# Kernel tuning notes

Measured on AMD Instinct MI355X. Metric: run time of the kernel, lower is better.

Reference implementation:

```python
import jax, jax.numpy as jnp
import numpy as np

NEG = -1000000000.0  # matches torch masked_fill value


def setup_inputs() -> dict:
    key = jax.random.key(0)
    ks = jax.random.split(key, 9)
    B, L, E = 2, 2048, 1024
    s = 0.02
    return {
        "query": jax.random.normal(ks[0], (B, L, E), dtype=jnp.float32),
        "w_q_w": jax.random.normal(ks[1], (E, E), dtype=jnp.float32) * s,
        "w_q_b": jax.random.normal(ks[2], (E,), dtype=jnp.float32) * s,
        "w_k_w": jax.random.normal(ks[3], (E, E), dtype=jnp.float32) * s,
        "w_k_b": jax.random.normal(ks[4], (E,), dtype=jnp.float32) * s,
        "w_v_w": jax.random.normal(ks[5], (E, E), dtype=jnp.float32) * s,
        "w_v_b": jax.random.normal(ks[6], (E,), dtype=jnp.float32) * s,
        "w_o_w": jax.random.normal(ks[7], (E, E), dtype=jnp.float32) * s,
        "w_o_b": jax.random.normal(ks[8], (E,), dtype=jnp.float32) * s,
    }


def reference(query, w_q_w, w_q_b, w_k_w, w_k_b, w_v_w, w_v_b, w_o_w, w_o_b):
    # self-attention: key = value = query (forward passes None for key/value)
    B, L, E = query.shape
    H = 16
    d_k = E // H
    scale = 1.0 / jnp.sqrt(jnp.float32(d_k))

    def proj(x, w, b):
        # torch Linear: x @ w.T + b ; then split heads -> [B, H, L, d_k]
        return (x @ w.T + b).reshape(B, L, H, d_k).transpose(0, 2, 1, 3)

    Q = proj(query, w_q_w, w_q_b)
    K = proj(query, w_k_w, w_k_b)
    V = proj(query, w_v_w, w_v_b)

    # full L x S score matrix, as in the eager original
    scores = jnp.einsum('bhqd,bhkd->bhqk', Q, K) * scale
    # causal attn_bias: upper triangle filled with -1e9 (is_causal=True path)
    causal = jnp.tril(jnp.ones((L, L), dtype=bool))
    scores = scores + jnp.where(causal, 0.0, NEG).astype(scores.dtype)
    # softmax, clear_nan (nan -> 0), + 1e-12 epsilon; dropout_p = 0.0 (no-op)
    attn = jnp.nan_to_num(jax.nn.softmax(scores, axis=-1), nan=0.0) + 1e-12

    ctx = jnp.einsum('bhqk,bhkd->bhqd', attn, V)  # [B,H,L,d_k]
    ctx = ctx.transpose(0, 2, 1, 3).reshape(B, L, E)
    return ctx @ w_o_w.T + w_o_b
```

## Files before the change

### kernel.cpp

```cpp
#include <hip/hip_runtime.h>
#include <hip/hip_bf16.h>
#include <math.h>

typedef __bf16 bf16;
typedef __bf16 bf16x4 __attribute__((ext_vector_type(4)));
typedef __bf16 bf16x8 __attribute__((ext_vector_type(8)));
typedef float  f32x4  __attribute__((ext_vector_type(4)));
typedef float  float4v __attribute__((ext_vector_type(4)));
typedef unsigned short u16x4 __attribute__((ext_vector_type(4)));

#define MFMA(a,b,c) __builtin_amdgcn_mfma_f32_16x16x32_bf16((a),(b),(c),0,0,0)

#define QSCALE 0.18033688011112042f
#define EXP2(x) __builtin_amdgcn_exp2f(x)

__device__ __forceinline__ void gload16(const bf16* g, bf16* l) {
  __builtin_amdgcn_global_load_lds(
      (const __attribute__((address_space(1))) void*)g,
      (__attribute__((address_space(3))) void*)l, 16, 0, 0);
}

__device__ __forceinline__ int detect_f32(const unsigned short* __restrict__ p) {
  int bad = 0;
  #pragma unroll
  for (int j = 0; j < 32; ++j) {
    const float x = __uint_as_float(((unsigned)p[j]) << 16);
    bad |= !(fabsf(x) <= 0.5f);
  }
  return bad;
}

__global__ void cvt_all_kernel(const void* x, const void* wq, const void* wk,
                               const void* wv, const void* wo,
                               const void* bq, const void* bk, const void* bv,
                               const void* bo,
                               bf16* cX, bf16* cWq, bf16* cWk, bf16* cWv,
                               bf16* cWo, bf16* cB)
{
  const int isf = detect_f32((const unsigned short*)bq);
  const int NX = 1048576, NW = 262144, NB = 256;
  const int total = NX + 4 * NW + 4 * NB;
  for (int gid = blockIdx.x * blockDim.x + threadIdx.x; gid < total;
       gid += gridDim.x * blockDim.x) {
    const void* s; bf16* d; int off;
    if (gid < NX)                { s = x;  d = cX;  off = gid; }
    else if (gid < NX + NW)      { s = wq; d = cWq; off = gid - NX; }
    else if (gid < NX + 2 * NW)  { s = wk; d = cWk; off = gid - NX - NW; }
    else if (gid < NX + 3 * NW)  { s = wv; d = cWv; off = gid - NX - 2 * NW; }
    else if (gid < NX + 4 * NW)  { s = wo; d = cWo; off = gid - NX - 3 * NW; }
    else {
      const int r = gid - NX - 4 * NW;
      const int wb = r / NB; off = r % NB;
      s = (wb == 0) ? bq : (wb == 1) ? bk : (wb == 2) ? bv : bo;
      d = cB + wb * 1024;
    }
    float4v v;
    if (isf) v = ((const float4v*)s)[off];
    else {
      u16x4 u = ((const u16x4*)s)[off];
      v = (float4v){__uint_as_float((unsigned)u.x << 16),
                    __uint_as_float((unsigned)u.y << 16),
                    __uint_as_float((unsigned)u.z << 16),
                    __uint_as_float((unsigned)u.w << 16)};
    }
    bf16x4 ov = {(bf16)v.x, (bf16)v.y, (bf16)v.z, (bf16)v.w};
    *(bf16x4*)&d[off * 4] = ov;
  }
}

static __device__ __forceinline__ void gemm128_core(
    const bf16* __restrict__ X, const bf16* __restrict__ W,
    int bm, int bn, f32x4 acc[4][4])
{
  __shared__ __align__(16) bf16 Als[128][64];
  __shared__ __align__(16) bf16 Bls[128][64];
  const int t    = threadIdx.x;
  const int lane = t & 63;
  const int w    = t >> 6;
  const int wr   = w >> 1, wc = w & 1;
  const int fr   = lane & 15;
  const int fq   = lane >> 4;
  const int lrow = lane >> 3;
  const int lcol = (lane & 7) * 8;

  #pragma unroll
  for (int m = 0; m < 4; ++m)
    #pragma unroll
    for (int n = 0; n < 4; ++n)
      acc[m][n] = (f32x4){0.f, 0.f, 0.f, 0.f};

  for (int k0 = 0; k0 < 1024; k0 += 64) {
    __syncthreads();
    #pragma unroll
    for (int p = 0; p < 4; ++p) {
      const int rb = p * 32 + w * 8;
      gload16(&X[(size_t)(bm + rb + lrow) * 1024 + k0 + lcol], &Als[rb][0]);
      gload16(&W[(size_t)(bn + rb + lrow) * 1024 + k0 + lcol], &Bls[rb][0]);
    }
    __syncthreads();
    #pragma unroll
    for (int kk = 0; kk < 64; kk += 32) {
      bf16x8 a[4], b[4];
      #pragma unroll
      for (int m = 0; m < 4; ++m)
        a[m] = *(const bf16x8*)&Als[wr * 64 + m * 16 + fr][kk + fq * 8];
      #pragma unroll
      for (int n = 0; n < 4; ++n)
        b[n] = *(const bf16x8*)&Bls[wc * 64 + n * 16 + fr][kk + fq * 8];
      __builtin_amdgcn_s_setprio(1);
      #pragma unroll
      for (int m = 0; m < 4; ++m)
        #pragma unroll
        for (int n = 0; n < 4; ++n)
          acc[m][n] = MFMA(a[m], b[n], acc[m][n]);
      __builtin_amdgcn_s_setprio(0);
    }
  }
}

__global__ __launch_bounds__(256, 3) void qkv_kernel(
    const bf16* __restrict__ X,
    const bf16* __restrict__ Wq, const bf16* __restrict__ Wk,
    const bf16* __restrict__ Wv, const bf16* __restrict__ Bias,
    bf16* __restrict__ Qo, bf16* __restrict__ Ko, bf16* __restrict__ Vto)
{
  const bf16 *W, *bias;
  bf16 *out;
  const int z = blockIdx.z;
  if (z == 0)      { W = Wq; bias = Bias;        out = Qo;  }
  else if (z == 1) { W = Wk; bias = Bias + 1024; out = Ko;  }
  else             { W = Wv; bias = Bias + 2048; out = Vto; }

  const int bm = blockIdx.x * 128, bn = blockIdx.y * 128;
  f32x4 acc[4][4];
  gemm128_core(X, W, bm, bn, acc);

  const int t = threadIdx.x, lane = t & 63, w = t >> 6;
  const int wr = w >> 1, wc = w & 1;
  const int fr = lane & 15, fq = lane >> 4;
  const float qs = (z == 0) ? QSCALE : 1.0f;

  #pragma unroll
  for (int n = 0; n < 4; ++n) {
    const int col = bn + wc * 64 + n * 16 + fr;
    const float bb = (float)bias[col];
    const int h = col >> 6, d = col & 63;
    if (z != 2) {
      #pragma unroll
      for (int m = 0; m < 4; ++m)
        #pragma unroll
        for (int r = 0; r < 4; ++r) {
          const int row = bm + wr * 64 + m * 16 + fq * 4 + r;
          const int b = row >> 11, li = row & 2047;
          out[(size_t)((b * 16 + h) * 2048 + li) * 64 + d] =
              (bf16)((acc[m][n][r] + bb) * qs);
        }
    } else {
      #pragma unroll
      for (int m = 0; m < 4; ++m) {
        const int tok0 = bm + wr * 64 + m * 16 + fq * 4;
        const int b = tok0 >> 11, li0 = tok0 & 2047;
        bf16x4 pk = {(bf16)(acc[m][n][0] + bb), (bf16)(acc[m][n][1] + bb),
                     (bf16)(acc[m][n][2] + bb), (bf16)(acc[m][n][3] + bb)};
        *(bf16x4*)&out[(size_t)((b * 16 + h) * 64 + d) * 2048 + li0] = pk;
      }
    }
  }
}

__device__ __forceinline__ f32x4 fmax4(f32x4 a, f32x4 b) {
  return (f32x4){fmaxf(a[0], b[0]), fmaxf(a[1], b[1]),
                 fmaxf(a[2], b[2]), fmaxf(a[3], b[3])};
}

__global__ __launch_bounds__(512, 4) void attn_kernel(
    const bf16* __restrict__ Q, const bf16* __restrict__ K,
    const bf16* __restrict__ Vt, bf16* __restrict__ CTX)
{
  const int bx = (int)blockIdx.x;
  const int gen = bx >> 8;
  const int u = bx & 255;
  const int bh = u >> 3;
  const int j = u & 7;
  const int qt = gen ? j : 15 - j;

  const int t = threadIdx.x, lane = t & 63, w = t >> 6;
  const int fr = lane & 15, fq = lane >> 4;
  const bf16* Qb = Q  + (size_t)bh * 2048 * 64;
  const bf16* Kb = K  + (size_t)bh * 2048 * 64;
  const bf16* Vb = Vt + (size_t)bh * 64 * 2048;
  const int q0 = qt * 128 + w * 16;
  const int myq = q0 + fr;
  const int nt = 2 * qt + 2;

  __shared__ __align__(16) bf16 Kls[2][64][64];
  __shared__ __align__(16) bf16 Vls[2][64][64];
  __shared__ __align__(16) bf16 Pls[8][16][64];

  const int X7   = (fr & 7) << 4;
  const int off0 = fr * 128 + ((fq * 16) ^ X7);
  const int off1 = fr * 128 + ((64 + fq * 16) ^ X7);
  const char* Kb0 = (const char*)Kls;
  const char* Vb0 = (const char*)Vls;
  char* Pw = (char*)Pls + w * 2048 + fr * 128;
  int pwoff[4];
  #pragma unroll
  for (int g = 0; g < 4; ++g) pwoff[g] = ((g * 32 + fq * 8) ^ X7);
  const int proff0 = ((fq * 16) ^ X7);
  const int proff1 = ((64 + fq * 16) ^ X7);

  const int r8 = lane >> 3;
  const int cb = (lane & 7) << 4;
  const int sc = (cb ^ (r8 << 4)) >> 1;
  const bf16* gk = Kb + (size_t)(w * 8 + r8) * 64 + sc;
  const bf16* gv = Vb + (size_t)(w * 8 + r8) * 2048 + sc;

  const bf16x8 qf0 = *(const bf16x8*)&Qb[(size_t)(q0 + fr) * 64 + fq * 8];
  const bf16x8 qf1 = *(const bf16x8*)&Qb[(size_t)(q0 + fr) * 64 + 32 + fq * 8];

  f32x4 o[4];
  #pragma unroll
  for (int g = 0; g < 4; ++g) o[g] = (f32x4){0.f, 0.f, 0.f, 0.f};
  float m_r = -1e30f;
  float s_part = 0.f;

  gload16(gk, &Kls[0][w * 8][0]);
  gload16(gv, &Vls[0][w * 8][0]);
  gk += 4096; gv += 64;
  __syncthreads();
  int cur = 0;

  for (int kt = 0; kt < nt; ++kt) {
    if (kt + 1 < nt) {
      gload16(gk, &Kls[cur ^ 1][w * 8][0]);
      gload16(gv, &Vls[cur ^ 1][w * 8][0]);
      gk += 4096; gv += 64;
    }

    const int kbase = kt * 64;
    if (kbase <= q0 + 15) {
      const char* kb = Kb0 + (cur << 13);
      const char* vb = Vb0 + (cur << 13);

      f32x4 S[4];
      __builtin_amdgcn_s_setprio(1);
      #pragma unroll
      for (int g = 0; g < 4; ++g) {
        bf16x8 kf0 = *(const bf16x8*)(kb + off0 + g * 2048);
        bf16x8 kf1 = *(const bf16x8*)(kb + off1 + g * 2048);
        f32x4 s = (f32x4){0.f, 0.f, 0.f, 0.f};
        s = MFMA(kf0, qf0, s);
        s = MFMA(kf1, qf1, s);
        S[g] = s;
      }
      __builtin_amdgcn_s_setprio(0);

      if (kbase + 63 > q0) {
        #pragma unroll
        for (int g = 0; g < 4; ++g)
          #pragma unroll
          for (int r = 0; r < 4; ++r)
            S[g][r] = (kbase + g * 16 + fq * 4 + r <= myq) ? S[g][r] : -1e9f;
      }
      f32x4 mv = fmax4(fmax4(S[0], S[1]), fmax4(S[2], S[3]));
      const float mxl = fmaxf(fmaxf(mv[0], mv[1]), fmaxf(mv[2], mv[3]));
      if (!__all(mxl <= m_r + 8.f)) {
        float mxq = fmaxf(mxl, __shfl_xor(mxl, 16));
        mxq = fmaxf(mxq, __shfl_xor(mxq, 32));
        const float mnew = fmaxf(m_r, mxq);
        const float f = EXP2(m_r - mnew);
        m_r = mnew;
        s_part *= f;
        float frow[4];
        #pragma unroll
        for (int r = 0; r < 4; ++r) frow[r] = __shfl(f, fq * 4 + r, 64);
        #pragma unroll
        for (int g = 0; g < 4; ++g)
          #pragma unroll
          for (int r = 0; r < 4; ++r) o[g][r] *= frow[r];
      }
      #pragma unroll
      for (int g = 0; g < 4; ++g)
        #pragma unroll
        for (int r = 0; r < 4; ++r) {
          const float p = EXP2(S[g][r] - m_r);
          S[g][r] = p;
          s_part += p;
        }
      #pragma unroll
      for (int g = 0; g < 4; ++g) {
        bf16x4 pk = {(bf16)S[g][0], (bf16)S[g][1], (bf16)S[g][2],
                     (bf16)S[g][3]};
        *(bf16x4*)(Pw + pwoff[g]) = pk;
      }
      __builtin_amdgcn_s_setprio(1);
      {
        bf16x8 pa0 = *(const bf16x8*)(Pw + proff0);
        #pragma unroll
        for (int g2 = 0; g2 < 4; ++g2) {
          bf16x8 vf = *(const bf16x8*)(vb + off0 + g2 * 2048);
          o[g2] = MFMA(pa0, vf, o[g2]);
        }
        bf16x8 pa1 = *(const bf16x8*)(Pw + proff1);
        #pragma unroll
        for (int g2 = 0; g2 < 4; ++g2) {
          bf16x8 vf = *(const bf16x8*)(vb + off1 + g2 * 2048);
          o[g2] = MFMA(pa1, vf, o[g2]);
        }
      }
      __builtin_amdgcn_s_setprio(0);
    }
    __syncthreads();
    cur ^= 1;
  }

  float s_r = s_part;
  s_r += __shfl_xor(s_r, 16);
  s_r += __shfl_xor(s_r, 32);
  const float inv = __builtin_amdgcn_rcpf(fmaxf(s_r, 1e-30f));
  float invr[4];
  #pragma unroll
  for (int r = 0; r < 4; ++r) invr[r] = __shfl(inv, fq * 4 + r, 64);
  const int b = bh >> 4, h = bh & 15;
  #pragma unroll
  for (int r = 0; r < 4; ++r) {
    const int tok = b * 2048 + q0 + fq * 4 + r;
    #pragma unroll
    for (int g2 = 0; g2 < 4; ++g2)
      CTX[(size_t)tok * 1024 + h * 64 + g2 * 16 + fr] =
          (bf16)(o[g2][r] * invr[r]);
  }
}

__global__ __launch_bounds__(256, 4) void out_kernel(
    const bf16* __restrict__ CTXi, const bf16* __restrict__ Wo,
    const bf16* __restrict__ bo, void* __restrict__ Y,
    const unsigned short* __restrict__ det)
{
  __shared__ __align__(16) bf16 Als[128][64];
  __shared__ __align__(16) bf16 Bls[64][64];
  const int isf = detect_f32(det);
  const int bm = blockIdx.x * 128, bn = blockIdx.y * 64;
  const int t = threadIdx.x, lane = t & 63, w = t >> 6;
  const int wr = w >> 1, wc = w & 1;
  const int fr = lane & 15, fq = lane >> 4;
  const int lrow = lane >> 3;
  const int lcol = (lane & 7) * 8;

  f32x4 acc[4][2];
  #pragma unroll
  for (int m = 0; m < 4; ++m)
    #pragma unroll
    for (int n = 0; n < 2; ++n)
      acc[m][n] = (f32x4){0.f, 0.f, 0.f, 0.f};

  for (int k0 = 0; k0 < 1024; k0 += 64) {
    __syncthreads();
    #pragma unroll
    for (int p = 0; p < 4; ++p) {
      const int rb = p * 32 + w * 8;
      gload16(&CTXi[(size_t)(bm + rb + lrow) * 1024 + k0 + lcol], &Als[rb][0]);
    }
    #pragma unroll
    for (int p = 0; p < 2; ++p) {
      const int rb = w * 16 + p * 8;
      gload16(&Wo[(size_t)(bn + rb + lrow) * 1024 + k0 + lcol], &Bls[rb][0]);
    }
    __syncthreads();
    #pragma unroll
    for (int kk = 0; kk < 64; kk += 32) {
      bf16x8 a[4], b[2];
      #pragma unroll
      for (int m = 0; m < 4; ++m)
        a[m] = *(const bf16x8*)&Als[wr * 64 + m * 16 + fr][kk + fq * 8];
      #pragma unroll
      for (int n = 0; n < 2; ++n)
        b[n] = *(const bf16x8*)&Bls[wc * 32 + n * 16 + fr][kk + fq * 8];
      __builtin_amdgcn_s_setprio(1);
      #pragma unroll
      for (int m = 0; m < 4; ++m)
        #pragma unroll
        for (int n = 0; n < 2; ++n)
          acc[m][n] = MFMA(a[m], b[n], acc[m][n]);
      __builtin_amdgcn_s_setprio(0);
    }
  }

  #pragma unroll
  for (int n = 0; n < 2; ++n) {
    const int col = bn + wc * 32 + n * 16 + fr;
    const float bb = (float)bo[col];
    #pragma unroll
    for (int m = 0; m < 4; ++m)
      #pragma unroll
      for (int r = 0; r < 4; ++r) {
        const int row = bm + wr * 64 + m * 16 + fq * 4 + r;
        const size_t idx = (size_t)row * 1024 + col;
        const float v = acc[m][n][r] + bb;
        if (isf) ((float*)Y)[idx] = v;
        else     ((bf16*)Y)[idx] = (bf16)v;
      }
  }
}

extern "C" void kernel_launch(void* const* d_in, const int* in_sizes, int n_in,
                              void* d_out, int out_size, void* d_ws, size_t ws_size,
                              hipStream_t stream) {
  char* ws = (char*)d_ws;
  const size_t MB = 1024 * 1024;

  bf16* cX  = (bf16*)(ws + 1 * MB);
  bf16* cWq = (bf16*)(ws + 9 * MB);
  bf16* cWk = (bf16*)(ws + 11 * MB);
  bf16* cWv = (bf16*)(ws + 13 * MB);
  bf16* cWo = (bf16*)(ws + 15 * MB);
  bf16* cB  = (bf16*)(ws + 17 * MB);
  bf16* Qw  = (bf16*)(ws + 18 * MB);
  bf16* Kw  = (bf16*)(ws + 26 * MB);
  bf16* Vt  = (bf16*)(ws + 34 * MB);
  bf16* CT  = (bf16*)(ws + 42 * MB);

  cvt_all_kernel<<<2048, 256, 0, stream>>>(d_in[0], d_in[1], d_in[3], d_in[5],
                                           d_in[7], d_in[2], d_in[4], d_in[6],
                                           d_in[8], cX, cWq, cWk, cWv, cWo, cB);

  qkv_kernel<<<dim3(32, 8, 3), 256, 0, stream>>>(cX, cWq, cWk, cWv, cB,
                                                 Qw, Kw, Vt);
  attn_kernel<<<512, 512, 0, stream>>>(Qw, Kw, Vt, CT);
  out_kernel<<<dim3(32, 16), 256, 0, stream>>>(CT, cWo, cB + 3072, d_out,
                                               (const unsigned short*)d_in[2]);
}
```

Before: 111.6 us.

## Split long causal attention rows across two blocks and merge partials

The attention kernel now uses 256-thread blocks over 64-query tiles. The 18 longest query tiles per head have their key range split in half across two blocks, which write unnormalized bf16 partial outputs plus running max and sum into workspace that is no longer needed. A new merge kernel rescales and combines the two partials into the context tensor. The aim is to shorten the critical path of the heaviest causal tiles and balance load across CUs, at the cost of an extra launch, partial-buffer traffic and bf16 rounding of the partials.

```diff
diff --git a/kernel.cpp b/kernel.cpp
--- a/kernel.cpp
+++ b/kernel.cpp
@@ -13,6 +13,9 @@
 
 #define QSCALE 0.18033688011112042f
 #define EXP2(x) __builtin_amdgcn_exp2f(x)
+
+#define PART_O_OFF   (1048576ull)
+#define PART_S_OFF   (1048576ull + 9437184ull)
 
 __device__ __forceinline__ void gload16(const bf16* g, bf16* l) {
   __builtin_amdgcn_global_load_lds(
@@ -173,29 +176,41 @@
                  fmaxf(a[2], b[2]), fmaxf(a[3], b[3])};
 }
 
-__global__ __launch_bounds__(512, 4) void attn_kernel(
+__global__ __launch_bounds__(256, 4) void attn_kernel(
     const bf16* __restrict__ Q, const bf16* __restrict__ K,
-    const bf16* __restrict__ Vt, bf16* __restrict__ CTX)
+    const bf16* __restrict__ Vt, bf16* __restrict__ CTX,
+    char* __restrict__ part)
 {
-  const int bx = (int)blockIdx.x;
-  const int gen = bx >> 8;
-  const int u = bx & 255;
-  const int bh = u >> 3;
-  const int j = u & 7;
-  const int qt = gen ? j : 15 - j;
+  const int id = (int)blockIdx.x;
+  int qt, bh, k0t, k1t, heavy;
+  if (id < 1152) {
+    const int pair = id >> 1, chunk = id & 1;
+    qt = 31 - (pair >> 5);
+    bh = pair & 31;
+    const int n = qt + 1, h = (n + 1) >> 1;
+    k0t = chunk ? h : 0;
+    k1t = chunk ? n : h;
+    heavy = 1;
+  } else {
+    const int r = id - 1152;
+    qt = 13 - (r >> 5);
+    bh = r & 31;
+    k0t = 0;
+    k1t = qt + 1;
+    heavy = 0;
+  }
 
   const int t = threadIdx.x, lane = t & 63, w = t >> 6;
   const int fr = lane & 15, fq = lane >> 4;
   const bf16* Qb = Q  + (size_t)bh * 2048 * 64;
   const bf16* Kb = K  + (size_t)bh * 2048 * 64;
   const bf16* Vb = Vt + (size_t)bh * 64 * 2048;
-  const int q0 = qt * 128 + w * 16;
+  const int q0 = qt * 64 + w * 16;
   const int myq = q0 + fr;
-  const int nt = 2 * qt + 2;
 
   __shared__ __align__(16) bf16 Kls[2][64][64];
   __shared__ __align__(16) bf16 Vls[2][64][64];
-  __shared__ __align__(16) bf16 Pls[8][16][64];
+  __shared__ __align__(16) bf16 Pls[4][16][64];
 
   const int X7   = (fr & 7) << 4;
   const int off0 = fr * 128 + ((fq * 16) ^ X7);
@@ -212,8 +227,10 @@
   const int r8 = lane >> 3;
   const int cb = (lane & 7) << 4;
   const int sc = (cb ^ (r8 << 4)) >> 1;
-  const bf16* gk = Kb + (size_t)(w * 8 + r8) * 64 + sc;
-  const bf16* gv = Vb + (size_t)(w * 8 + r8) * 2048 + sc;
+  const bf16* gk0 = Kb + (size_t)(k0t * 64 + w * 8 + r8) * 64 + sc;
+  const bf16* gk1 = gk0 + 32 * 64;
+  const bf16* gv0 = Vb + (size_t)(w * 8 + r8) * 2048 + k0t * 64 + sc;
+  const bf16* gv1 = gv0 + (size_t)32 * 2048;
 
   const bf16x8 qf0 = *(const bf16x8*)&Qb[(size_t)(q0 + fr) * 64 + fq * 8];
   const bf16x8 qf1 = *(const bf16x8*)&Qb[(size_t)(q0 + fr) * 64 + 32 + fq * 8];
@@ -224,92 +241,94 @@
   float m_r = -1e30f;
   float s_part = 0.f;
 
-  gload16(gk, &Kls[0][w * 8][0]);
-  gload16(gv, &Vls[0][w * 8][0]);
-  gk += 4096; gv += 64;
+  gload16(gk0, &Kls[0][w * 8][0]);
+  gload16(gk1, &Kls[0][32 + w * 8][0]);
+  gload16(gv0, &Vls[0][w * 8][0]);
+  gload16(gv1, &Vls[0][32 + w * 8][0]);
+  gk0 += 4096; gk1 += 4096; gv0 += 64; gv1 += 64;
   __syncthreads();
   int cur = 0;
 
-  for (int kt = 0; kt < nt; ++kt) {
-    if (kt + 1 < nt) {
-      gload16(gk, &Kls[cur ^ 1][w * 8][0]);
-      gload16(gv, &Vls[cur ^ 1][w * 8][0]);
-      gk += 4096; gv += 64;
-    }
-
-    const int kbase = kt * 64;
-    if (kbase <= q0 + 15) {
-      const char* kb = Kb0 + (cur << 13);
-      const char* vb = Vb0 + (cur << 13);
-
-      f32x4 S[4];
-      __builtin_amdgcn_s_setprio(1);
-      #pragma unroll
-      for (int g = 0; g < 4; ++g) {
-        bf16x8 kf0 = *(const bf16x8*)(kb + off0 + g * 2048);
-        bf16x8 kf1 = *(const bf16x8*)(kb + off1 + g * 2048);
-        f32x4 s = (f32x4){0.f, 0.f, 0.f, 0.f};
-        s = MFMA(kf0, qf0, s);
-        s = MFMA(kf1, qf1, s);
-        S[g] = s;
-      }
-      __builtin_amdgcn_s_setprio(0);
-
-      if (kbase + 63 > q0) {
-        #pragma unroll
-        for (int g = 0; g < 4; ++g)
-          #pragma unroll
-          for (int r = 0; r < 4; ++r)
-            S[g][r] = (kbase + g * 16 + fq * 4 + r <= myq) ? S[g][r] : -1e9f;
-      }
-      f32x4 mv = fmax4(fmax4(S[0], S[1]), fmax4(S[2], S[3]));
-      const float mxl = fmaxf(fmaxf(mv[0], mv[1]), fmaxf(mv[2], mv[3]));
-      if (!__all(mxl <= m_r + 8.f)) {
-        float mxq = fmaxf(mxl, __shfl_xor(mxl, 16));
-        mxq = fmaxf(mxq, __shfl_xor(mxq, 32));
-        const float mnew = fmaxf(m_r, mxq);
-        const float f = EXP2(m_r - mnew);
-        m_r = mnew;
-        s_part *= f;
-        float frow[4];
-        #pragma unroll
-        for (int r = 0; r < 4; ++r) frow[r] = __shfl(f, fq * 4 + r, 64);
-        #pragma unroll
-        for (int g = 0; g < 4; ++g)
-          #pragma unroll
-          for (int r = 0; r < 4; ++r) o[g][r] *= frow[r];
-      }
+  for (int kt = k0t; kt < k1t; ++kt) {
+    if (kt + 1 < k1t) {
+      bf16 (*Kn)[64] = Kls[cur ^ 1];
+      bf16 (*Vn)[64] = Vls[cur ^ 1];
+      gload16(gk0, &Kn[w * 8][0]);
+      gload16(gk1, &Kn[32 + w * 8][0]);
+      gload16(gv0, &Vn[w * 8][0]);
+      gload16(gv1, &Vn[32 + w * 8][0]);
+      gk0 += 4096; gk1 += 4096; gv0 += 64; gv1 += 64;
+    }
+
+    const char* kb = Kb0 + (cur << 13);
+    const char* vb = Vb0 + (cur << 13);
+
+    f32x4 S[4];
+    __builtin_amdgcn_s_setprio(1);
+    #pragma unroll
+    for (int g = 0; g < 4; ++g) {
+      bf16x8 kf0 = *(const bf16x8*)(kb + off0 + g * 2048);
+      bf16x8 kf1 = *(const bf16x8*)(kb + off1 + g * 2048);
+      f32x4 s = (f32x4){0.f, 0.f, 0.f, 0.f};
+      s = MFMA(kf0, qf0, s);
+      s = MFMA(kf1, qf1, s);
+      S[g] = s;
+    }
+    __builtin_amdgcn_s_setprio(0);
+
+    if (kt == qt) {
       #pragma unroll
       for (int g = 0; g < 4; ++g)
         #pragma unroll
-        for (int r = 0; r < 4; ++r) {
-          const float p = EXP2(S[g][r] - m_r);
-          S[g][r] = p;
-          s_part += p;
-        }
-      #pragma unroll
-      for (int g = 0; g < 4; ++g) {
-        bf16x4 pk = {(bf16)S[g][0], (bf16)S[g][1], (bf16)S[g][2],
-                     (bf16)S[g][3]};
-        *(bf16x4*)(Pw + pwoff[g]) = pk;
+        for (int r = 0; r < 4; ++r)
+          S[g][r] = (kt * 64 + g * 16 + fq * 4 + r <= myq) ? S[g][r] : -1e9f;
+    }
+    f32x4 mv = fmax4(fmax4(S[0], S[1]), fmax4(S[2], S[3]));
+    const float mxl = fmaxf(fmaxf(mv[0], mv[1]), fmaxf(mv[2], mv[3]));
+    if (!__all(mxl <= m_r + 8.f)) {
+      float mxq = fmaxf(mxl, __shfl_xor(mxl, 16));
+      mxq = fmaxf(mxq, __shfl_xor(mxq, 32));
+      const float mnew = fmaxf(m_r, mxq);
+      const float f = EXP2(m_r - mnew);
+      m_r = mnew;
+      s_part *= f;
+      float frow[4];
+      #pragma unroll
+      for (int r = 0; r < 4; ++r) frow[r] = __shfl(f, fq * 4 + r, 64);
+      #pragma unroll
+      for (int g = 0; g < 4; ++g)
+        #pragma unroll
+        for (int r = 0; r < 4; ++r) o[g][r] *= frow[r];
+    }
+    #pragma unroll
+    for (int g = 0; g < 4; ++g)
+      #pragma unroll
+      for (int r = 0; r < 4; ++r) {
+        const float p = EXP2(S[g][r] - m_r);
+        S[g][r] = p;
+        s_part += p;
       }
-      __builtin_amdgcn_s_setprio(1);
-      {
-        bf16x8 pa0 = *(const bf16x8*)(Pw + proff0);
-        #pragma unroll
-        for (int g2 = 0; g2 < 4; ++g2) {
-          bf16x8 vf = *(const bf16x8*)(vb + off0 + g2 * 2048);
-          o[g2] = MFMA(pa0, vf, o[g2]);
-        }
-        bf16x8 pa1 = *(const bf16x8*)(Pw + proff1);
-        #pragma unroll
-        for (int g2 = 0; g2 < 4; ++g2) {
-          bf16x8 vf = *(const bf16x8*)(vb + off1 + g2 * 2048);
-          o[g2] = MFMA(pa1, vf, o[g2]);
-        }
+    #pragma unroll
+    for (int g = 0; g < 4; ++g) {
+      bf16x4 pk = {(bf16)S[g][0], (bf16)S[g][1], (bf16)S[g][2], (bf16)S[g][3]};
+      *(bf16x4*)(Pw + pwoff[g]) = pk;
+    }
+    __builtin_amdgcn_s_setprio(1);
+    {
+      bf16x8 pa0 = *(const bf16x8*)(Pw + proff0);
+      #pragma unroll
+      for (int g2 = 0; g2 < 4; ++g2) {
+        bf16x8 vf = *(const bf16x8*)(vb + off0 + g2 * 2048);
+        o[g2] = MFMA(pa0, vf, o[g2]);
       }
-      __builtin_amdgcn_s_setprio(0);
-    }
+      bf16x8 pa1 = *(const bf16x8*)(Pw + proff1);
+      #pragma unroll
+      for (int g2 = 0; g2 < 4; ++g2) {
+        bf16x8 vf = *(const bf16x8*)(vb + off1 + g2 * 2048);
+        o[g2] = MFMA(pa1, vf, o[g2]);
+      }
+    }
+    __builtin_amdgcn_s_setprio(0);
     __syncthreads();
     cur ^= 1;
   }
@@ -317,18 +336,74 @@
   float s_r = s_part;
   s_r += __shfl_xor(s_r, 16);
   s_r += __shfl_xor(s_r, 32);
-  const float inv = __builtin_amdgcn_rcpf(fmaxf(s_r, 1e-30f));
-  float invr[4];
-  #pragma unroll
-  for (int r = 0; r < 4; ++r) invr[r] = __shfl(inv, fq * 4 + r, 64);
+
+  if (heavy) {
+    char* op = part + PART_O_OFF + (size_t)id * 8192 + t * 32;
+    #pragma unroll
+    for (int g2 = 0; g2 < 4; ++g2) {
+      bf16x4 pk = {(bf16)o[g2][0], (bf16)o[g2][1], (bf16)o[g2][2],
+                   (bf16)o[g2][3]};
+      *(bf16x4*)(op + g2 * 8) = pk;
+    }
+    float2 st = {m_r, s_r};
+    *(float2*)(part + PART_S_OFF + (size_t)id * 2048 + t * 8) = st;
+  } else {
+    const float inv = __builtin_amdgcn_rcpf(fmaxf(s_r, 1e-30f));
+    float invr[4];
+    #pragma unroll
+    for (int r = 0; r < 4; ++r) invr[r] = __shfl(inv, fq * 4 + r, 64);
+    const int b = bh >> 4, h = bh & 15;
+    #pragma unroll
+    for (int r = 0; r < 4; ++r) {
+      const int tok = b * 2048 + q0 + fq * 4 + r;
+      #pragma unroll
+      for (int g2 = 0; g2 < 4; ++g2)
+        CTX[(size_t)tok * 1024 + h * 64 + g2 * 16 + fr] =
+            (bf16)(o[g2][r] * invr[r]);
+    }
+  }
+}
+
+__global__ __launch_bounds__(256, 8) void merge_kernel(
+    const char* __restrict__ part, bf16* __restrict__ CTX)
+{
+  const int bi = (int)blockIdx.x;
+  const int qt = 31 - (bi >> 5), bh = bi & 31;
+  const int t = threadIdx.x, lane = t & 63, w = t >> 6;
+  const int fr = lane & 15, fq = lane >> 4;
+  const int s0 = bi * 2, s1 = s0 + 1;
+
+  const float2 st0 = *(const float2*)(part + PART_S_OFF + (size_t)s0 * 2048 + t * 8);
+  const float2 st1 = *(const float2*)(part + PART_S_OFF + (size_t)s1 * 2048 + t * 8);
+  const float M  = fmaxf(st0.x, st1.x);
+  const float f0 = EXP2(st0.x - M);
+  const float f1 = EXP2(st1.x - M);
+  const float ssum = st0.y * f0 + st1.y * f1;
+  const float inv = __builtin_amdgcn_rcpf(fmaxf(ssum, 1e-30f));
+  const float a0 = f0 * inv, a1 = f1 * inv;
+
+  float a0r[4], a1r[4];
+  #pragma unroll
+  for (int r = 0; r < 4; ++r) {
+    a0r[r] = __shfl(a0, fq * 4 + r, 64);
+    a1r[r] = __shfl(a1, fq * 4 + r, 64);
+  }
+
+  const char* o0p = part + PART_O_OFF + (size_t)s0 * 8192 + t * 32;
+  const char* o1p = part + PART_O_OFF + (size_t)s1 * 8192 + t * 32;
+
   const int b = bh >> 4, h = bh & 15;
-  #pragma unroll
-  for (int r = 0; r < 4; ++r) {
-    const int tok = b * 2048 + q0 + fq * 4 + r;
-    #pragma unroll
-    for (int g2 = 0; g2 < 4; ++g2)
-      CTX[(size_t)tok * 1024 + h * 64 + g2 * 16 + fr] =
-          (bf16)(o[g2][r] * invr[r]);
+  const int q0 = qt * 64 + w * 16;
+  #pragma unroll
+  for (int g2 = 0; g2 < 4; ++g2) {
+    bf16x4 p0 = *(const bf16x4*)(o0p + g2 * 8);
+    bf16x4 p1 = *(const bf16x4*)(o1p + g2 * 8);
+    #pragma unroll
+    for (int r = 0; r < 4; ++r) {
+      const float v = (float)p0[r] * a0r[r] + (float)p1[r] * a1r[r];
+      const int tok = b * 2048 + q0 + fq * 4 + r;
+      CTX[(size_t)tok * 1024 + h * 64 + g2 * 16 + fr] = (bf16)v;
+    }
   }
 }
 
@@ -426,7 +501,8 @@
 
   qkv_kernel<<<dim3(32, 8, 3), 256, 0, stream>>>(cX, cWq, cWk, cWv, cB,
                                                  Qw, Kw, Vt);
-  attn_kernel<<<512, 512, 0, stream>>>(Qw, Kw, Vt, CT);
+  attn_kernel<<<1600, 256, 0, stream>>>(Qw, Kw, Vt, CT, ws);
+  merge_kernel<<<576, 256, 0, stream>>>(ws, CT);
   out_kernel<<<dim3(32, 16), 256, 0, stream>>>(CT, cWo, cB + 3072, d_out,
                                                (const unsigned short*)d_in[2]);
 }
```

After: 113.7 us. About the same (+1.9%).

## Rewrite attention with 32x32 MFMA, register-resident P, and smaller blocks

Applied to the files above, without the earlier changes.

The attention kernel now uses 32x32x16 bf16 MFMA with each wave owning 32 query rows, and blocks shrink to 2 waves covering 64 queries, which doubles the grid to 1024 blocks. The softmax probabilities are repacked in registers with cvt_pk_bf16 and a cross-half lane shuffle instead of going through an LDS round-trip. Causal tile skipping is handled per 32-key half. Work balancing is reordered over four generations of query tiles. This cuts LDS traffic and per-key-tile overhead but raises register pressure and shuffle work, and each block now stages K/V for fewer queries.

```diff
diff --git a/kernel.cpp b/kernel.cpp
--- a/kernel.cpp
+++ b/kernel.cpp
@@ -6,10 +6,13 @@
 typedef __bf16 bf16x4 __attribute__((ext_vector_type(4)));
 typedef __bf16 bf16x8 __attribute__((ext_vector_type(8)));
 typedef float  f32x4  __attribute__((ext_vector_type(4)));
+typedef float  f32x16 __attribute__((ext_vector_type(16)));
 typedef float  float4v __attribute__((ext_vector_type(4)));
 typedef unsigned short u16x4 __attribute__((ext_vector_type(4)));
-
-#define MFMA(a,b,c) __builtin_amdgcn_mfma_f32_16x16x32_bf16((a),(b),(c),0,0,0)
+typedef unsigned int   u32x4 __attribute__((ext_vector_type(4)));
+
+#define MFMA16(a,b,c) __builtin_amdgcn_mfma_f32_16x16x32_bf16((a),(b),(c),0,0,0)
+#define MFMA32(a,b,c) __builtin_amdgcn_mfma_f32_32x32x16_bf16((a),(b),(c),0,0,0)
 
 #define QSCALE 0.18033688011112042f
 #define EXP2(x) __builtin_amdgcn_exp2f(x)
@@ -18,6 +21,12 @@
   __builtin_amdgcn_global_load_lds(
       (const __attribute__((address_space(1))) void*)g,
       (__attribute__((address_space(3))) void*)l, 16, 0, 0);
+}
+
+__device__ __forceinline__ unsigned cvt_pk_bf16(float lo, float hi) {
+  unsigned r;
+  asm("v_cvt_pk_bf16_f32 %0, %1, %2" : "=v"(r) : "v"(lo), "v"(hi));
+  return r;
 }
 
 __device__ __forceinline__ int detect_f32(const unsigned short* __restrict__ p) {
@@ -112,7 +121,7 @@
       for (int m = 0; m < 4; ++m)
         #pragma unroll
         for (int n = 0; n < 4; ++n)
-          acc[m][n] = MFMA(a[m], b[n], acc[m][n]);
+          acc[m][n] = MFMA16(a[m], b[n], acc[m][n]);
       __builtin_amdgcn_s_setprio(0);
     }
   }
@@ -168,12 +177,7 @@
   }
 }
 
-__device__ __forceinline__ f32x4 fmax4(f32x4 a, f32x4 b) {
-  return (f32x4){fmaxf(a[0], b[0]), fmaxf(a[1], b[1]),
-                 fmaxf(a[2], b[2]), fmaxf(a[3], b[3])};
-}
-
-__global__ __launch_bounds__(512, 4) void attn_kernel(
+__global__ __launch_bounds__(128, 3) void attn_kernel(
     const bf16* __restrict__ Q, const bf16* __restrict__ K,
     const bf16* __restrict__ Vt, bf16* __restrict__ CTX)
 {
@@ -182,153 +186,220 @@
   const int u = bx & 255;
   const int bh = u >> 3;
   const int j = u & 7;
-  const int qt = gen ? j : 15 - j;
+  int qt;
+  if (gen == 0)      qt = 31 - j;
+  else if (gen == 1) qt = 16 + j;
+  else if (gen == 2) qt = 15 - j;
+  else               qt = j;
 
   const int t = threadIdx.x, lane = t & 63, w = t >> 6;
-  const int fr = lane & 15, fq = lane >> 4;
+  const int l31 = lane & 31, ishi = lane >> 5;
   const bf16* Qb = Q  + (size_t)bh * 2048 * 64;
   const bf16* Kb = K  + (size_t)bh * 2048 * 64;
   const bf16* Vb = Vt + (size_t)bh * 64 * 2048;
-  const int q0 = qt * 128 + w * 16;
-  const int myq = q0 + fr;
-  const int nt = 2 * qt + 2;
+  const int q0w = qt * 64 + w * 32;
+  const int myq = q0w + l31;
+  const int nt = qt + 1;
+  const int hi4 = ishi * 4;
 
   __shared__ __align__(16) bf16 Kls[2][64][64];
   __shared__ __align__(16) bf16 Vls[2][64][64];
-  __shared__ __align__(16) bf16 Pls[8][16][64];
-
-  const int X7   = (fr & 7) << 4;
-  const int off0 = fr * 128 + ((fq * 16) ^ X7);
-  const int off1 = fr * 128 + ((64 + fq * 16) ^ X7);
-  const char* Kb0 = (const char*)Kls;
-  const char* Vb0 = (const char*)Vls;
-  char* Pw = (char*)Pls + w * 2048 + fr * 128;
-  int pwoff[4];
-  #pragma unroll
-  for (int g = 0; g < 4; ++g) pwoff[g] = ((g * 32 + fq * 8) ^ X7);
-  const int proff0 = ((fq * 16) ^ X7);
-  const int proff1 = ((64 + fq * 16) ^ X7);
+
+  const int koff[16] = {0,1,2,3, 8,9,10,11, 16,17,18,19, 24,25,26,27};
+
+  const int X7 = (l31 & 7) << 4;
+  const char* Kbase = (const char*)Kls + (size_t)l31 * 128;
+  const char* Vbase = (const char*)Vls + (size_t)l31 * 128;
+  int kcol[4];
+  #pragma unroll
+  for (int c = 0; c < 4; ++c) kcol[c] = (32 * c + 16 * ishi) ^ X7;
+  int vcol[2][2];
+  #pragma unroll
+  for (int kt2 = 0; kt2 < 2; ++kt2)
+    #pragma unroll
+    for (int ch = 0; ch < 2; ++ch)
+      vcol[kt2][ch] = (kt2 * 64 + ch * 32 + 16 * ishi) ^ X7;
 
   const int r8 = lane >> 3;
-  const int cb = (lane & 7) << 4;
-  const int sc = (cb ^ (r8 << 4)) >> 1;
-  const bf16* gk = Kb + (size_t)(w * 8 + r8) * 64 + sc;
-  const bf16* gv = Vb + (size_t)(w * 8 + r8) * 2048 + sc;
-
-  const bf16x8 qf0 = *(const bf16x8*)&Qb[(size_t)(q0 + fr) * 64 + fq * 8];
-  const bf16x8 qf1 = *(const bf16x8*)&Qb[(size_t)(q0 + fr) * 64 + 32 + fq * 8];
-
-  f32x4 o[4];
-  #pragma unroll
-  for (int g = 0; g < 4; ++g) o[g] = (f32x4){0.f, 0.f, 0.f, 0.f};
-  float m_r = -1e30f;
-  float s_part = 0.f;
-
-  gload16(gk, &Kls[0][w * 8][0]);
-  gload16(gv, &Vls[0][w * 8][0]);
-  gk += 4096; gv += 64;
+  const int slot = lane & 7;
+  const bf16* gk[4];
+  const bf16* gv[4];
+  #pragma unroll
+  for (int s = 0; s < 4; ++s) {
+    const int rs = s * 16 + w * 8 + r8;
+    const int sc = ((slot * 16) ^ ((rs & 7) << 4)) >> 1;
+    gk[s] = Kb + (size_t)rs * 64 + sc;
+    gv[s] = Vb + (size_t)rs * 2048 + sc;
+  }
+
+  bf16x8 qf[4];
+  #pragma unroll
+  for (int c = 0; c < 4; ++c)
+    qf[c] = *(const bf16x8*)&Qb[(size_t)myq * 64 + c * 16 + ishi * 8];
+
+  f32x16 o0, o1;
+  #pragma unroll
+  for (int i = 0; i < 16; ++i) { o0[i] = 0.f; o1[i] = 0.f; }
+  float m_r = -1e30f, s_part = 0.f;
+
+  #pragma unroll
+  for (int s = 0; s < 4; ++s) {
+    gload16(gk[s], &Kls[0][s * 16 + w * 8][0]);
+    gload16(gv[s], &Vls[0][s * 16 + w * 8][0]);
+    gk[s] += 4096; gv[s] += 64;
+  }
   __syncthreads();
   int cur = 0;
 
   for (int kt = 0; kt < nt; ++kt) {
     if (kt + 1 < nt) {
-      gload16(gk, &Kls[cur ^ 1][w * 8][0]);
-      gload16(gv, &Vls[cur ^ 1][w * 8][0]);
-      gk += 4096; gv += 64;
-    }
-
+      #pragma unroll
+      for (int s = 0; s < 4; ++s) {
+        gload16(gk[s], &Kls[cur ^ 1][s * 16 + w * 8][0]);
+        gload16(gv[s], &Vls[cur ^ 1][s * 16 + w * 8][0]);
+        gk[s] += 4096; gv[s] += 64;
+      }
+    }
+    const char* kb = Kbase + (cur << 13);
+    const char* vb = Vbase + (cur << 13);
     const int kbase = kt * 64;
-    if (kbase <= q0 + 15) {
-      const char* kb = Kb0 + (cur << 13);
-      const char* vb = Vb0 + (cur << 13);
-
-      f32x4 S[4];
-      __builtin_amdgcn_s_setprio(1);
-      #pragma unroll
-      for (int g = 0; g < 4; ++g) {
-        bf16x8 kf0 = *(const bf16x8*)(kb + off0 + g * 2048);
-        bf16x8 kf1 = *(const bf16x8*)(kb + off1 + g * 2048);
-        f32x4 s = (f32x4){0.f, 0.f, 0.f, 0.f};
-        s = MFMA(kf0, qf0, s);
-        s = MFMA(kf1, qf1, s);
-        S[g] = s;
-      }
-      __builtin_amdgcn_s_setprio(0);
-
-      if (kbase + 63 > q0) {
-        #pragma unroll
-        for (int g = 0; g < 4; ++g)
-          #pragma unroll
-          for (int r = 0; r < 4; ++r)
-            S[g][r] = (kbase + g * 16 + fq * 4 + r <= myq) ? S[g][r] : -1e9f;
-      }
-      f32x4 mv = fmax4(fmax4(S[0], S[1]), fmax4(S[2], S[3]));
-      const float mxl = fmaxf(fmaxf(mv[0], mv[1]), fmaxf(mv[2], mv[3]));
-      if (!__all(mxl <= m_r + 8.f)) {
-        float mxq = fmaxf(mxl, __shfl_xor(mxl, 16));
-        mxq = fmaxf(mxq, __shfl_xor(mxq, 32));
-        const float mnew = fmaxf(m_r, mxq);
-        const float f = EXP2(m_r - mnew);
-        m_r = mnew;
-        s_part *= f;
-        float frow[4];
-        #pragma unroll
-        for (int r = 0; r < 4; ++r) frow[r] = __shfl(f, fq * 4 + r, 64);
-        #pragma unroll
-        for (int g = 0; g < 4; ++g)
-          #pragma unroll
-          for (int r = 0; r < 4; ++r) o[g][r] *= frow[r];
-      }
-      #pragma unroll
-      for (int g = 0; g < 4; ++g)
-        #pragma unroll
-        for (int r = 0; r < 4; ++r) {
-          const float p = EXP2(S[g][r] - m_r);
-          S[g][r] = p;
-          s_part += p;
+    const bool vis1 = (kbase + 32 <= q0w + 31);
+
+    f32x16 S0, S1;
+    __builtin_amdgcn_s_setprio(1);
+    {
+      f32x16 z;
+      #pragma unroll
+      for (int i = 0; i < 16; ++i) z[i] = 0.f;
+      S0 = z;
+      #pragma unroll
+      for (int c = 0; c < 4; ++c) {
+        bf16x8 kf = *(const bf16x8*)(kb + kcol[c]);
+        S0 = MFMA32(kf, qf[c], S0);
+      }
+      if (vis1) {
+        S1 = z;
+        #pragma unroll
+        for (int c = 0; c < 4; ++c) {
+          bf16x8 kf = *(const bf16x8*)(kb + 4096 + kcol[c]);
+          S1 = MFMA32(kf, qf[c], S1);
         }
-      #pragma unroll
-      for (int g = 0; g < 4; ++g) {
-        bf16x4 pk = {(bf16)S[g][0], (bf16)S[g][1], (bf16)S[g][2],
-                     (bf16)S[g][3]};
-        *(bf16x4*)(Pw + pwoff[g]) = pk;
-      }
-      __builtin_amdgcn_s_setprio(1);
-      {
-        bf16x8 pa0 = *(const bf16x8*)(Pw + proff0);
-        #pragma unroll
-        for (int g2 = 0; g2 < 4; ++g2) {
-          bf16x8 vf = *(const bf16x8*)(vb + off0 + g2 * 2048);
-          o[g2] = MFMA(pa0, vf, o[g2]);
+      }
+    }
+    __builtin_amdgcn_s_setprio(0);
+
+    if (kt == qt) {
+      if (kbase + 31 > q0w) {
+        #pragma unroll
+        for (int i = 0; i < 16; ++i)
+          S0[i] = (kbase + koff[i] + hi4 <= myq) ? S0[i] : -1e9f;
+      }
+      if (vis1 && kbase + 63 > q0w) {
+        #pragma unroll
+        for (int i = 0; i < 16; ++i)
+          S1[i] = (kbase + 32 + koff[i] + hi4 <= myq) ? S1[i] : -1e9f;
+      }
+    }
+
+    float mxl = -1e30f;
+    #pragma unroll
+    for (int i = 0; i < 16; ++i) mxl = fmaxf(mxl, S0[i]);
+    if (vis1) {
+      #pragma unroll
+      for (int i = 0; i < 16; ++i) mxl = fmaxf(mxl, S1[i]);
+    }
+    if (!__all(mxl <= m_r + 8.f)) {
+      float mxq = fmaxf(mxl, __shfl_xor(mxl, 32));
+      const float mnew = fmaxf(m_r, mxq);
+      const float f = EXP2(m_r - mnew);
+      m_r = mnew;
+      s_part *= f;
+      #pragma unroll
+      for (int i = 0; i < 16; ++i) {
+        const float fb = __shfl(f, koff[i] + hi4, 64);
+        o0[i] *= fb; o1[i] *= fb;
+      }
+    }
+
+    __builtin_amdgcn_s_setprio(1);
+    {
+      #pragma unroll
+      for (int i = 0; i < 16; ++i) {
+        const float p = EXP2(S0[i] - m_r);
+        S0[i] = p; s_part += p;
+      }
+      unsigned dA[4], dB[4];
+      #pragma unroll
+      for (int p4 = 0; p4 < 4; ++p4) {
+        dA[p4] = cvt_pk_bf16(S0[4 * p4 + 0], S0[4 * p4 + 1]);
+        dB[p4] = cvt_pk_bf16(S0[4 * p4 + 2], S0[4 * p4 + 3]);
+      }
+      #pragma unroll
+      for (int ch = 0; ch < 2; ++ch) {
+        const unsigned ownA = ishi ? dA[2 * ch + 1] : dA[2 * ch];
+        const unsigned ownB = ishi ? dB[2 * ch + 1] : dB[2 * ch];
+        const unsigned sndA = ishi ? dA[2 * ch]     : dA[2 * ch + 1];
+        const unsigned sndB = ishi ? dB[2 * ch]     : dB[2 * ch + 1];
+        const unsigned rcvA = (unsigned)__shfl_xor((int)sndA, 32, 64);
+        const unsigned rcvB = (unsigned)__shfl_xor((int)sndB, 32, 64);
+        u32x4 au;
+        au.x = ishi ? rcvA : ownA;
+        au.y = ishi ? rcvB : ownB;
+        au.z = ishi ? ownA : rcvA;
+        au.w = ishi ? ownB : rcvB;
+        const bf16x8 af = __builtin_bit_cast(bf16x8, au);
+        bf16x8 vf0 = *(const bf16x8*)(vb + vcol[0][ch]);
+        bf16x8 vf1 = *(const bf16x8*)(vb + 4096 + vcol[0][ch]);
+        o0 = MFMA32(af, vf0, o0);
+        o1 = MFMA32(af, vf1, o1);
+      }
+      if (vis1) {
+        #pragma unroll
+        for (int i = 0; i < 16; ++i) {
+          const float p = EXP2(S1[i] - m_r);
+          S1[i] = p; s_part += p;
         }
-        bf16x8 pa1 = *(const bf16x8*)(Pw + proff1);
-        #pragma unroll
-        for (int g2 = 0; g2 < 4; ++g2) {
-          bf16x8 vf = *(const bf16x8*)(vb + off1 + g2 * 2048);
-          o[g2] = MFMA(pa1, vf, o[g2]);
+        #pragma unroll
+        for (int p4 = 0; p4 < 4; ++p4) {
+          dA[p4] = cvt_pk_bf16(S1[4 * p4 + 0], S1[4 * p4 + 1]);
+          dB[p4] = cvt_pk_bf16(S1[4 * p4 + 2], S1[4 * p4 + 3]);
         }
-      }
-      __builtin_amdgcn_s_setprio(0);
-    }
+        #pragma unroll
+        for (int ch = 0; ch < 2; ++ch) {
+          const unsigned ownA = ishi ? dA[2 * ch + 1] : dA[2 * ch];
+          const unsigned ownB = ishi ? dB[2 * ch + 1] : dB[2 * ch];
+          const unsigned sndA = ishi ? dA[2 * ch]     : dA[2 * ch + 1];
+          const unsigned sndB = ishi ? dB[2 * ch]     : dB[2 * ch + 1];
+          const unsigned rcvA = (unsigned)__shfl_xor((int)sndA, 32, 64);
+          const unsigned rcvB = (unsigned)__shfl_xor((int)sndB, 32, 64);
+          u32x4 au;
+          au.x = ishi ? rcvA : ownA;
+          au.y = ishi ? rcvB : ownB;
+          au.z = ishi ? ownA : rcvA;
+          au.w = ishi ? ownB : rcvB;
+          const bf16x8 af = __builtin_bit_cast(bf16x8, au);
+          bf16x8 vf0 = *(const bf16x8*)(vb + vcol[1][ch]);
+          bf16x8 vf1 = *(const bf16x8*)(vb + 4096 + vcol[1][ch]);
+          o0 = MFMA32(af, vf0, o0);
+          o1 = MFMA32(af, vf1, o1);
+        }
+      }
+    }
+    __builtin_amdgcn_s_setprio(0);
     __syncthreads();
     cur ^= 1;
   }
 
-  float s_r = s_part;
-  s_r += __shfl_xor(s_r, 16);
-  s_r += __shfl_xor(s_r, 32);
+  float s_r = s_part + __shfl_xor(s_part, 32);
   const float inv = __builtin_amdgcn_rcpf(fmaxf(s_r, 1e-30f));
-  float invr[4];
-  #pragma unroll
-  for (int r = 0; r < 4; ++r) invr[r] = __shfl(inv, fq * 4 + r, 64);
   const int b = bh >> 4, h = bh & 15;
   #pragma unroll
-  for (int r = 0; r < 4; ++r) {
-    const int tok = b * 2048 + q0 + fq * 4 + r;
-    #pragma unroll
-    for (int g2 = 0; g2 < 4; ++g2)
-      CTX[(size_t)tok * 1024 + h * 64 + g2 * 16 + fr] =
-          (bf16)(o[g2][r] * invr[r]);
+  for (int i = 0; i < 16; ++i) {
+    const int rowq = koff[i] + hi4;
+    const float iv = __shfl(inv, rowq, 64);
+    const int tok = b * 2048 + q0w + rowq;
+    CTX[(size_t)tok * 1024 + h * 64 + l31]      = (bf16)(o0[i] * iv);
+    CTX[(size_t)tok * 1024 + h * 64 + 32 + l31] = (bf16)(o1[i] * iv);
   }
 }
 
@@ -381,7 +452,7 @@
       for (int m = 0; m < 4; ++m)
         #pragma unroll
         for (int n = 0; n < 2; ++n)
-          acc[m][n] = MFMA(a[m], b[n], acc[m][n]);
+          acc[m][n] = MFMA16(a[m], b[n], acc[m][n]);
       __builtin_amdgcn_s_setprio(0);
     }
   }
@@ -426,7 +497,7 @@
 
   qkv_kernel<<<dim3(32, 8, 3), 256, 0, stream>>>(cX, cWq, cWk, cWv, cB,
                                                  Qw, Kw, Vt);
-  attn_kernel<<<512, 512, 0, stream>>>(Qw, Kw, Vt, CT);
+  attn_kernel<<<1024, 128, 0, stream>>>(Qw, Kw, Vt, CT);
   out_kernel<<<dim3(32, 16), 256, 0, stream>>>(CT, cWo, cB + 3072, d_out,
                                                (const unsigned short*)d_in[2]);
 }
```

Result: slower. 118.4 us (+6.1%).

## Shrink attention query tile to 64 rows with 4 waves and 1024 blocks

Applied to the files above, without the earlier changes.

The attention kernel now processes 64-query tiles with 256 threads (4 waves) per block, launching 1024 blocks scheduled heaviest-first across four generations. Each thread loads two K/V rows per tile, and the per-wave skip of fully masked key tiles is dropped because a 64-query tile matches the 64-key tile granularity. The goal is better load balance and occupancy on the causal triangle with less wasted work per block. In exchange, K/V tiles are reloaded from global memory twice as often per query row, and each block synchronises more often relative to its compute.

```diff
diff --git a/kernel.cpp b/kernel.cpp
--- a/kernel.cpp
+++ b/kernel.cpp
@@ -173,7 +173,7 @@
                  fmaxf(a[2], b[2]), fmaxf(a[3], b[3])};
 }
 
-__global__ __launch_bounds__(512, 4) void attn_kernel(
+__global__ __launch_bounds__(256, 4) void attn_kernel(
     const bf16* __restrict__ Q, const bf16* __restrict__ K,
     const bf16* __restrict__ Vt, bf16* __restrict__ CTX)
 {
@@ -182,20 +182,24 @@
   const int u = bx & 255;
   const int bh = u >> 3;
   const int j = u & 7;
-  const int qt = gen ? j : 15 - j;
+  int qt;
+  if (gen == 0)      qt = 31 - j;
+  else if (gen == 1) qt = 16 + j;
+  else if (gen == 2) qt = 15 - j;
+  else               qt = j;
 
   const int t = threadIdx.x, lane = t & 63, w = t >> 6;
   const int fr = lane & 15, fq = lane >> 4;
   const bf16* Qb = Q  + (size_t)bh * 2048 * 64;
   const bf16* Kb = K  + (size_t)bh * 2048 * 64;
   const bf16* Vb = Vt + (size_t)bh * 64 * 2048;
-  const int q0 = qt * 128 + w * 16;
+  const int q0 = qt * 64 + w * 16;
   const int myq = q0 + fr;
-  const int nt = 2 * qt + 2;
+  const int nt = qt + 1;
 
   __shared__ __align__(16) bf16 Kls[2][64][64];
   __shared__ __align__(16) bf16 Vls[2][64][64];
-  __shared__ __align__(16) bf16 Pls[8][16][64];
+  __shared__ __align__(16) bf16 Pls[4][16][64];
 
   const int X7   = (fr & 7) << 4;
   const int off0 = fr * 128 + ((fq * 16) ^ X7);
@@ -212,8 +216,10 @@
   const int r8 = lane >> 3;
   const int cb = (lane & 7) << 4;
   const int sc = (cb ^ (r8 << 4)) >> 1;
-  const bf16* gk = Kb + (size_t)(w * 8 + r8) * 64 + sc;
-  const bf16* gv = Vb + (size_t)(w * 8 + r8) * 2048 + sc;
+  const bf16* gk0 = Kb + (size_t)(w * 8 + r8) * 64 + sc;
+  const bf16* gk1 = Kb + (size_t)(32 + w * 8 + r8) * 64 + sc;
+  const bf16* gv0 = Vb + (size_t)(w * 8 + r8) * 2048 + sc;
+  const bf16* gv1 = Vb + (size_t)(32 + w * 8 + r8) * 2048 + sc;
 
   const bf16x8 qf0 = *(const bf16x8*)&Qb[(size_t)(q0 + fr) * 64 + fq * 8];
   const bf16x8 qf1 = *(const bf16x8*)&Qb[(size_t)(q0 + fr) * 64 + 32 + fq * 8];
@@ -224,92 +230,94 @@
   float m_r = -1e30f;
   float s_part = 0.f;
 
-  gload16(gk, &Kls[0][w * 8][0]);
-  gload16(gv, &Vls[0][w * 8][0]);
-  gk += 4096; gv += 64;
+  gload16(gk0, &Kls[0][w * 8][0]);
+  gload16(gk1, &Kls[0][32 + w * 8][0]);
+  gload16(gv0, &Vls[0][w * 8][0]);
+  gload16(gv1, &Vls[0][32 + w * 8][0]);
+  gk0 += 4096; gk1 += 4096; gv0 += 64; gv1 += 64;
   __syncthreads();
   int cur = 0;
 
   for (int kt = 0; kt < nt; ++kt) {
     if (kt + 1 < nt) {
-      gload16(gk, &Kls[cur ^ 1][w * 8][0]);
-      gload16(gv, &Vls[cur ^ 1][w * 8][0]);
-      gk += 4096; gv += 64;
-    }
-
-    const int kbase = kt * 64;
-    if (kbase <= q0 + 15) {
-      const char* kb = Kb0 + (cur << 13);
-      const char* vb = Vb0 + (cur << 13);
-
-      f32x4 S[4];
-      __builtin_amdgcn_s_setprio(1);
-      #pragma unroll
-      for (int g = 0; g < 4; ++g) {
-        bf16x8 kf0 = *(const bf16x8*)(kb + off0 + g * 2048);
-        bf16x8 kf1 = *(const bf16x8*)(kb + off1 + g * 2048);
-        f32x4 s = (f32x4){0.f, 0.f, 0.f, 0.f};
-        s = MFMA(kf0, qf0, s);
-        s = MFMA(kf1, qf1, s);
-        S[g] = s;
-      }
-      __builtin_amdgcn_s_setprio(0);
-
-      if (kbase + 63 > q0) {
-        #pragma unroll
-        for (int g = 0; g < 4; ++g)
-          #pragma unroll
-          for (int r = 0; r < 4; ++r)
-            S[g][r] = (kbase + g * 16 + fq * 4 + r <= myq) ? S[g][r] : -1e9f;
-      }
-      f32x4 mv = fmax4(fmax4(S[0], S[1]), fmax4(S[2], S[3]));
-      const float mxl = fmaxf(fmaxf(mv[0], mv[1]), fmaxf(mv[2], mv[3]));
-      if (!__all(mxl <= m_r + 8.f)) {
-        float mxq = fmaxf(mxl, __shfl_xor(mxl, 16));
-        mxq = fmaxf(mxq, __shfl_xor(mxq, 32));
-        const float mnew = fmaxf(m_r, mxq);
-        const float f = EXP2(m_r - mnew);
-        m_r = mnew;
-        s_part *= f;
-        float frow[4];
-        #pragma unroll
-        for (int r = 0; r < 4; ++r) frow[r] = __shfl(f, fq * 4 + r, 64);
-        #pragma unroll
-        for (int g = 0; g < 4; ++g)
-          #pragma unroll
-          for (int r = 0; r < 4; ++r) o[g][r] *= frow[r];
-      }
+      bf16 (*Kn)[64] = Kls[cur ^ 1];
+      bf16 (*Vn)[64] = Vls[cur ^ 1];
+      gload16(gk0, &Kn[w * 8][0]);
+      gload16(gk1, &Kn[32 + w * 8][0]);
+      gload16(gv0, &Vn[w * 8][0]);
+      gload16(gv1, &Vn[32 + w * 8][0]);
+      gk0 += 4096; gk1 += 4096; gv0 += 64; gv1 += 64;
+    }
+
+    const char* kb = Kb0 + (cur << 13);
+    const char* vb = Vb0 + (cur << 13);
+
+    f32x4 S[4];
+    __builtin_amdgcn_s_setprio(1);
+    #pragma unroll
+    for (int g = 0; g < 4; ++g) {
+      bf16x8 kf0 = *(const bf16x8*)(kb + off0 + g * 2048);
+      bf16x8 kf1 = *(const bf16x8*)(kb + off1 + g * 2048);
+      f32x4 s = (f32x4){0.f, 0.f, 0.f, 0.f};
+      s = MFMA(kf0, qf0, s);
+      s = MFMA(kf1, qf1, s);
+      S[g] = s;
+    }
+    __builtin_amdgcn_s_setprio(0);
+
+    if (kt == qt) {
       #pragma unroll
       for (int g = 0; g < 4; ++g)
         #pragma unroll
-        for (int r = 0; r < 4; ++r) {
-          const float p = EXP2(S[g][r] - m_r);
-          S[g][r] = p;
-          s_part += p;
-        }
-      #pragma unroll
-      for (int g = 0; g < 4; ++g) {
-        bf16x4 pk = {(bf16)S[g][0], (bf16)S[g][1], (bf16)S[g][2],
-                     (bf16)S[g][3]};
-        *(bf16x4*)(Pw + pwoff[g]) = pk;
+        for (int r = 0; r < 4; ++r)
+          S[g][r] = (kt * 64 + g * 16 + fq * 4 + r <= myq) ? S[g][r] : -1e9f;
+    }
+    f32x4 mv = fmax4(fmax4(S[0], S[1]), fmax4(S[2], S[3]));
+    const float mxl = fmaxf(fmaxf(mv[0], mv[1]), fmaxf(mv[2], mv[3]));
+    if (!__all(mxl <= m_r + 8.f)) {
+      float mxq = fmaxf(mxl, __shfl_xor(mxl, 16));
+      mxq = fmaxf(mxq, __shfl_xor(mxq, 32));
+      const float mnew = fmaxf(m_r, mxq);
+      const float f = EXP2(m_r - mnew);
+      m_r = mnew;
+      s_part *= f;
+      float frow[4];
+      #pragma unroll
+      for (int r = 0; r < 4; ++r) frow[r] = __shfl(f, fq * 4 + r, 64);
+      #pragma unroll
+      for (int g = 0; g < 4; ++g)
+        #pragma unroll
+        for (int r = 0; r < 4; ++r) o[g][r] *= frow[r];
+    }
+    #pragma unroll
+    for (int g = 0; g < 4; ++g)
+      #pragma unroll
+      for (int r = 0; r < 4; ++r) {
+        const float p = EXP2(S[g][r] - m_r);
+        S[g][r] = p;
+        s_part += p;
       }
-      __builtin_amdgcn_s_setprio(1);
-      {
-        bf16x8 pa0 = *(const bf16x8*)(Pw + proff0);
-        #pragma unroll
-        for (int g2 = 0; g2 < 4; ++g2) {
-          bf16x8 vf = *(const bf16x8*)(vb + off0 + g2 * 2048);
-          o[g2] = MFMA(pa0, vf, o[g2]);
-        }
-        bf16x8 pa1 = *(const bf16x8*)(Pw + proff1);
-        #pragma unroll
-        for (int g2 = 0; g2 < 4; ++g2) {
-          bf16x8 vf = *(const bf16x8*)(vb + off1 + g2 * 2048);
-          o[g2] = MFMA(pa1, vf, o[g2]);
-        }
+    #pragma unroll
+    for (int g = 0; g < 4; ++g) {
+      bf16x4 pk = {(bf16)S[g][0], (bf16)S[g][1], (bf16)S[g][2], (bf16)S[g][3]};
+      *(bf16x4*)(Pw + pwoff[g]) = pk;
+    }
+    __builtin_amdgcn_s_setprio(1);
+    {
+      bf16x8 pa0 = *(const bf16x8*)(Pw + proff0);
+      #pragma unroll
+      for (int g2 = 0; g2 < 4; ++g2) {
+        bf16x8 vf = *(const bf16x8*)(vb + off0 + g2 * 2048);
+        o[g2] = MFMA(pa0, vf, o[g2]);
       }
-      __builtin_amdgcn_s_setprio(0);
-    }
+      bf16x8 pa1 = *(const bf16x8*)(Pw + proff1);
+      #pragma unroll
+      for (int g2 = 0; g2 < 4; ++g2) {
+        bf16x8 vf = *(const bf16x8*)(vb + off1 + g2 * 2048);
+        o[g2] = MFMA(pa1, vf, o[g2]);
+      }
+    }
+    __builtin_amdgcn_s_setprio(0);
     __syncthreads();
     cur ^= 1;
   }
@@ -426,7 +434,7 @@
 
   qkv_kernel<<<dim3(32, 8, 3), 256, 0, stream>>>(cX, cWq, cWk, cWv, cB,
                                                  Qw, Kw, Vt);
-  attn_kernel<<<512, 512, 0, stream>>>(Qw, Kw, Vt, CT);
+  attn_kernel<<<1024, 256, 0, stream>>>(Qw, Kw, Vt, CT);
   out_kernel<<<dim3(32, 16), 256, 0, stream>>>(CT, cWo, cB + 3072, d_out,
                                                (const unsigned short*)d_in[2]);
 }
```

New measurement: 110.4 us. About the same (-1.1%).
